# Kernel tuning notes

Measured on AMD Instinct MI355X. Metric: run time of the kernel, lower is better.

Reference implementation:

```python
import jax, jax.numpy as jnp
import numpy as np

EPS = 1e-5
SLOPE = 0.01  # LeakyReLU negative_slope

def _ln(x, g, b):
    m = jnp.mean(x, axis=-1, keepdims=True)
    v = jnp.mean((x - m) ** 2, axis=-1, keepdims=True)
    return (x - m) * jax.lax.rsqrt(v + EPS) * g + b

def _lrelu(x):
    return jnp.where(x >= 0, x, SLOPE * x)

def _s6(x, W1, b1, W2, b2, W3, b3, A):
    # x: (B, L, D); A: (D, N). Mamba-style S6 selective scan.
    Bm = x @ W2 + b2                       # (B, L, N) input-dependent B
    Cm = x @ W3 + b3                       # (B, L, N) input-dependent C
    delta = jax.nn.softplus(x @ W1 + b1)   # (B, L, D) step sizes
    dA = jnp.exp(jnp.einsum('bld,dn->bldn', delta, A))            # (B,L,D,N)
    dBx = jnp.einsum('bld,bln->bldn', delta, Bm) * x[..., None]    # (B,L,D,N) dB * x
    Bsz, L, D = x.shape
    N = A.shape[1]
    def step(h, inp):
        dA_t, dBx_t, C_t = inp
        h = dA_t * h + dBx_t                       # (B, D, N)
        return h, jnp.einsum('bn,bdn->bd', C_t, h)  # y_t: (B, D)
    xs = (jnp.transpose(dA, (1, 0, 2, 3)),
          jnp.transpose(dBx, (1, 0, 2, 3)),
          jnp.transpose(Cm, (1, 0, 2)))
    _, ys = jax.lax.scan(step, jnp.zeros((Bsz, D, N), x.dtype), xs)
    return jnp.transpose(ys, (1, 0, 2))  # (B, L, D)

def _fwd(text, audio, video, tW1, tb1, tg1, tbe1, tW2, tb2, tg2, tbe2, sW1, sb1, sW2, sb2, sW3, sb3, sA, aW1, ab1, ag1, abe1, aW2, ab2, ag2, abe2, vW1, vb1, vg1, vbe1, vW2, vb2, vg2, vbe2, cW1, cb1, cW2, cb2):
    # text branch: Linear+LN+LeakyReLU x2, Dropout(eval=identity), S6
    t = _lrelu(_ln(text @ tW1 + tb1, tg1, tbe1))
    t = _lrelu(_ln(t @ tW2 + tb2, tg2, tbe2))
    t = _s6(t, sW1, sb1, sW2, sb2, sW3, sb3, sA)
    # audio / video branches are computed but do not feed the output (as in source)
    a = _lrelu(_ln(audio @ aW1 + ab1, ag1, abe1))
    a = _lrelu(_ln(a @ aW2 + ab2, ag2, abe2))
    v = _lrelu(_ln(video @ vW1 + vb1, vg1, vbe1))
    v = _lrelu(_ln(v @ vW2 + vb2, vg2, vbe2))
    o1 = t @ cW1 + cb1
    return o1 @ cW2 + cb2  # (B, L, 2)

def setup_inputs() -> dict:
    key = jax.random.key(0)
    ks = iter(jax.random.split(key, 64))
    def W(shape, s=0.05):
        return jax.random.normal(next(ks), shape, jnp.float32) * s
    B, L = 64, 63
    d = {
        'text': jax.random.normal(next(ks), (B, L, 100), jnp.float32),
        'audio': jax.random.normal(next(ks), (B, L, 73), jnp.float32),
        'video': jax.random.normal(next(ks), (B, L, 100), jnp.float32),
        'tW1': W((100, 128)), 'tb1': jnp.zeros(128), 'tg1': jnp.ones(128), 'tbe1': jnp.zeros(128),
        'tW2': W((128, 100)), 'tb2': jnp.zeros(100), 'tg2': jnp.ones(100), 'tbe2': jnp.zeros(100),
        'sW1': W((100, 100)), 'sb1': jnp.zeros(100),
        'sW2': W((100, 300)), 'sb2': jnp.zeros(300),
        'sW3': W((100, 300)), 'sb3': jnp.zeros(300),
        'sA': jnp.full((100, 300), 1.0 / np.sqrt(300.0), jnp.float32),  # F.normalize(ones, dim=-1)
        'aW1': W((73, 256)), 'ab1': jnp.zeros(256), 'ag1': jnp.ones(256), 'abe1': jnp.zeros(256),
        'aW2': W((256, 100)), 'ab2': jnp.zeros(100), 'ag2': jnp.ones(100), 'abe2': jnp.zeros(100),
        'vW1': W((100, 256)), 'vb1': jnp.zeros(256), 'vg1': jnp.ones(256), 'vbe1': jnp.zeros(256),
        'vW2': W((256, 100)), 'vb2': jnp.zeros(100), 'vg2': jnp.ones(100), 'vbe2': jnp.zeros(100),
        'cW1': W((100, 50)), 'cb1': jnp.zeros(50),
        'cW2': W((50, 2)), 'cb2': jnp.zeros(2),
    }
    return d

def reference(text, audio, video, tW1, tb1, tg1, tbe1, tW2, tb2, tg2, tbe2, sW1, sb1, sW2, sb2, sW3, sb3, sA, aW1, ab1, ag1, abe1, aW2, ab2, ag2, abe2, vW1, vb1, vg1, vbe1, vW2, vb2, vg2, vbe2, cW1, cb1, cW2, cb2):
    return _fwd(text, audio, video, tW1, tb1, tg1, tbe1, tW2, tb2, tg2, tbe2, sW1, sb1, sW2, sb2, sW3, sb3, sA, aW1, ab1, ag1, abe1, aW2, ab2, ag2, abe2, vW1, vb1, vg1, vbe1, vW2, vb2, vg2, vbe2, cW1, cb1, cW2, cb2)
```

## Files before the change

kernel.cpp:

```cpp
#include <hip/hip_runtime.h>
#include <hip/hip_bf16.h>


typedef __hip_bfloat16 bf16;

#define BATCH 64
#define SEQ   63
#define ROWS  (BATCH * SEQ)
#define DIN   100
#define H1    128
#define DM    100
#define NS    300

__device__ __forceinline__ float2 up2(unsigned u) {
    float2 r;
    r.x = __uint_as_float(u << 16);
    r.y = __uint_as_float(u & 0xffff0000u);
    return r;
}
template<bool ISB>
__device__ __forceinline__ float LD(const void* p, int i) {
    if (ISB) return __bfloat162float(((const bf16*)p)[i]);
    else     return ((const float*)p)[i];
}
template<bool ISB>
__device__ __forceinline__ float2 LD2(const void* p, int i) {
    if (ISB) return up2(((const unsigned*)p)[i]);
    else     return ((const float2*)p)[i];
}
__device__ __forceinline__ float waveReduceSum(float v) {
#pragma unroll
    for (int off = 32; off > 0; off >>= 1) v += __shfl_xor(v, off, 64);
    return v;
}
__device__ __forceinline__ float4 waveReduceSum4(float4 v) {
#pragma unroll
    for (int off = 32; off > 0; off >>= 1) {
        const float a = __shfl_xor(v.x, off, 64);
        const float b = __shfl_xor(v.y, off, 64);
        const float c = __shfl_xor(v.z, off, 64);
        const float d = __shfl_xor(v.w, off, 64);
        v.x += a; v.y += b; v.z += c; v.w += d;
    }
    return v;
}
__device__ __forceinline__ float lrelu(float x) { return x >= 0.f ? x : 0.01f * x; }
__device__ __forceinline__ float softplusf(float x) {
    return (x > 20.f) ? x : log1pf(__expf(x));
}
__device__ __forceinline__ bool flags_uniform(const float* __restrict__ f) {
    bool u = true;
#pragma unroll
    for (int i = 0; i < 8; ++i) u &= (f[i] > 0.5f);
    return u;
}
__device__ __forceinline__ bool detect_bf16(const unsigned short* __restrict__ probe) {
    const int l = threadIdx.x & 63;
    const unsigned u0 = probe[l * 2];
    const unsigned u1 = probe[l * 2 + 1];
    const float v0 = fabsf(__uint_as_float(u0 << 16));
    const float v1 = fabsf(__uint_as_float(u1 << 16));
    const bool big = !(v0 < 1000.f) || !(v1 < 1000.f);
    const bool zero_even = (u0 == 0u);
    const unsigned long long mb = __ballot(big);
    const unsigned long long mz = __ballot(zero_even);
    return (mb == 0ULL) && (__popcll(mz) < 32);
}

template<bool ISB>
__device__ __forceinline__ void a_main(
    const void* __restrict__ text,
    const void* __restrict__ tW1, const void* __restrict__ tb1,
    const void* __restrict__ tg1, const void* __restrict__ tbe1,
    const void* __restrict__ tW2, const void* __restrict__ tb2,
    const void* __restrict__ tg2, const void* __restrict__ tbe2,
    const void* __restrict__ sW1w, const void* __restrict__ sb1,
    float* __restrict__ ddx, float* __restrict__ t2g,
    float* __restrict__ sW,
    float (&xb)[4][DIN][2], float (&t1b)[4][H1][2], float (&t2b)[4][DM][2])
{
    const int tid  = threadIdx.x;
    const int w    = tid >> 6;
    const int lane = tid & 63;
    const int r0   = blockIdx.x * 8 + w * 2;

    if (lane < 50) {
#pragma unroll
        for (int r = 0; r < 2; ++r) {
            const float2 xv = LD2<ISB>(text, (r0 + r) * 50 + lane);
            xb[w][2 * lane][r]     = xv.x;
            xb[w][2 * lane + 1][r] = xv.y;
        }
    }
    for (int i = tid; i < 6400; i += 256)
        *(float2*)&sW[2 * i] = LD2<ISB>(tW1, i);
    __syncthreads();

    const float2 b1v = LD2<ISB>(tb1, lane);
    float ax0 = b1v.x, ay0 = b1v.y, ax1 = b1v.x, ay1 = b1v.y;
#pragma unroll 10
    for (int k = 0; k < DIN; ++k) {
        const float2 wv = *(const float2*)&sW[k * 128 + 2 * lane];
        const float2 xv = *(const float2*)&xb[w][k][0];
        ax0 += xv.x * wv.x; ay0 += xv.x * wv.y;
        ax1 += xv.y * wv.x; ay1 += xv.y * wv.y;
    }
    {
        float4 red = waveReduceSum4(make_float4(
            ax0 + ay0, ax0 * ax0 + ay0 * ay0,
            ax1 + ay1, ax1 * ax1 + ay1 * ay1));
        const float m0 = red.x * (1.f / 128.f);
        const float rs0 = rsqrtf(red.y * (1.f / 128.f) - m0 * m0 + 1e-5f);
        const float m1 = red.z * (1.f / 128.f);
        const float rs1 = rsqrtf(red.w * (1.f / 128.f) - m1 * m1 + 1e-5f);
        const float2 g = LD2<ISB>(tg1, lane), be = LD2<ISB>(tbe1, lane);
        float2 v;
        v.x = lrelu((ax0 - m0) * rs0 * g.x + be.x);
        v.y = lrelu((ax1 - m1) * rs1 * g.x + be.x);
        *(float2*)&t1b[w][2 * lane][0] = v;
        v.x = lrelu((ay0 - m0) * rs0 * g.y + be.y);
        v.y = lrelu((ay1 - m1) * rs1 * g.y + be.y);
        *(float2*)&t1b[w][2 * lane + 1][0] = v;
    }
    __syncthreads();

    for (int i = tid; i < 6400; i += 256)
        *(float2*)&sW[2 * i] = LD2<ISB>(tW2, i);
    __syncthreads();

    const bool act = lane < 50;
    const int  li  = act ? lane : 0;
    const float2 b2v = LD2<ISB>(tb2, li);
    float cx0 = b2v.x, cy0 = b2v.y, cx1 = b2v.x, cy1 = b2v.y;
#pragma unroll 8
    for (int k = 0; k < H1; ++k) {
        const float2 wv = *(const float2*)&sW[k * 100 + 2 * li];
        const float2 tv = *(const float2*)&t1b[w][k][0];
        cx0 += tv.x * wv.x; cy0 += tv.x * wv.y;
        cx1 += tv.y * wv.x; cy1 += tv.y * wv.y;
    }
    float u0x, u0y, u1x, u1y;
    {
        float4 red = waveReduceSum4(act ? make_float4(
            cx0 + cy0, cx0 * cx0 + cy0 * cy0,
            cx1 + cy1, cx1 * cx1 + cy1 * cy1) : make_float4(0.f, 0.f, 0.f, 0.f));
        const float m0 = red.x * 0.01f;
        const float rs0 = rsqrtf(red.y * 0.01f - m0 * m0 + 1e-5f);
        const float m1 = red.z * 0.01f;
        const float rs1 = rsqrtf(red.w * 0.01f - m1 * m1 + 1e-5f);
        if (act) {
            const float2 g = LD2<ISB>(tg2, lane), be = LD2<ISB>(tbe2, lane);
            u0x = lrelu((cx0 - m0) * rs0 * g.x + be.x);
            u0y = lrelu((cy0 - m0) * rs0 * g.y + be.y);
            u1x = lrelu((cx1 - m1) * rs1 * g.x + be.x);
            u1y = lrelu((cy1 - m1) * rs1 * g.y + be.y);
            t2b[w][2 * lane][0] = u0x; t2b[w][2 * lane + 1][0] = u0y;
            t2b[w][2 * lane][1] = u1x; t2b[w][2 * lane + 1][1] = u1y;
            *(float2*)(t2g + (r0)     * DM + 2 * lane) = make_float2(u0x, u0y);
            *(float2*)(t2g + (r0 + 1) * DM + 2 * lane) = make_float2(u1x, u1y);
        }
    }
    __syncthreads();

    for (int i = tid; i < 5000; i += 256)
        *(float2*)&sW[2 * i] = LD2<ISB>(sW1w, i);
    __syncthreads();

    const float2 sbv = LD2<ISB>(sb1, li);
    float dA0x = sbv.x, dA0y = sbv.y, dA1x = sbv.x, dA1y = sbv.y;
#pragma unroll 10
    for (int k = 0; k < DM; ++k) {
        const float2 wv = *(const float2*)&sW[k * 100 + 2 * li];
        const float2 tv = *(const float2*)&t2b[w][k][0];
        dA0x += tv.x * wv.x; dA0y += tv.x * wv.y;
        dA1x += tv.y * wv.x; dA1y += tv.y * wv.y;
    }
    if (act) {
        float de0 = softplusf(dA0x), de1 = softplusf(dA0y);
        float4 o;
        o.x = de0; o.y = de0 * u0x; o.z = de1; o.w = de1 * u0y;
        *(float4*)(ddx + (r0) * (2 * DM) + 4 * lane) = o;
        de0 = softplusf(dA1x); de1 = softplusf(dA1y);
        o.x = de0; o.y = de0 * u1x; o.z = de1; o.w = de1 * u1y;
        *(float4*)(ddx + (r0 + 1) * (2 * DM) + 4 * lane) = o;
    }
}

template<bool ISB>
__device__ __forceinline__ void a_prep(
    const void* __restrict__ sW2, const void* __restrict__ sb2,
    const void* __restrict__ sW3, const void* __restrict__ sb3,
    float* __restrict__ M33p, float* __restrict__ k0w, float* __restrict__ sW,
    int d3)
{
    const int tid = threadIdx.x;
    const int w = tid >> 6, lane = tid & 63;
    float* W3row = sW;
    float* b2v   = sW + 320;
    float* b3v   = sW + 640;
    for (int i = tid; i < 300; i += 256) {
        W3row[i] = LD<ISB>(sW3, d3 * 300 + i);
        b2v[i]   = LD<ISB>(sb2, i);
        b3v[i]   = LD<ISB>(sb3, i);
    }
    __syncthreads();
    for (int g = 0; g < 6; ++g) {
        const int d2 = w * 25 + g * 4;
        float4 p = make_float4(0.f, 0.f, 0.f, 0.f);
#pragma unroll
        for (int rep = 0; rep < 5; ++rep) {
            const int n = lane + 64 * rep;
            if (n < 300) {
                const float w3 = W3row[n];
                p.x += LD<ISB>(sW2, (d2 + 0) * 300 + n) * w3;
                p.y += LD<ISB>(sW2, (d2 + 1) * 300 + n) * w3;
                p.z += LD<ISB>(sW2, (d2 + 2) * 300 + n) * w3;
                p.w += LD<ISB>(sW2, (d2 + 3) * 300 + n) * w3;
            }
        }
        p = waveReduceSum4(p);
        if (lane == 0) {
            M33p[d3 * 102 + d2 + 0] = p.x;
            M33p[d3 * 102 + d2 + 1] = p.y;
            M33p[d3 * 102 + d2 + 2] = p.z;
            M33p[d3 * 102 + d2 + 3] = p.w;
        }
    }
    {
        const int d2 = w * 25 + 24;
        float4 p = make_float4(0.f, 0.f, 0.f, 0.f);
#pragma unroll
        for (int rep = 0; rep < 5; ++rep) {
            const int n = lane + 64 * rep;
            if (n < 300) {
                p.x += LD<ISB>(sW2, d2 * 300 + n) * W3row[n];
                if (w == 0) p.y += W3row[n] * b2v[n];
                if (w == 1) p.y += LD<ISB>(sW2, d3 * 300 + n) * b3v[n];
                if (w == 2 && d3 == 0) p.y += b2v[n] * b3v[n];
            }
        }
        p = waveReduceSum4(p);
        if (lane == 0) {
            M33p[d3 * 102 + d2] = p.x;
            if (w == 0) M33p[d3 * 102 + 100] = p.y;
            if (w == 1) M33p[d3 * 102 + 101] = p.y;
            if (w == 2 && d3 == 0) k0w[0] = p.y;
        }
    }
}

template<bool ISB>
__device__ __forceinline__ void a_check(
    const void* __restrict__ sA, float* __restrict__ Afl,
    float* __restrict__ sW, int j)
{
    const int tid = threadIdx.x;
    const float a0 = LD<ISB>(sA, 0);
    bool ok = true;
    for (int i = j * 3750 + tid; i < (j + 1) * 3750; i += 256)
        ok &= (LD<ISB>(sA, i) == a0);
    if (tid == 0) sW[960] = 1.f;
    __syncthreads();
    if (!ok) sW[960] = 0.f;
    __syncthreads();
    if (tid == 0) Afl[j] = sW[960];
    if (j == 0 && tid == 1) Afl[8] = a0;
}

template<bool ISB>
__device__ __forceinline__ void a_mkv(
    const void* __restrict__ cW1, const void* __restrict__ cb1,
    const void* __restrict__ cW2, const void* __restrict__ cb2,
    float* __restrict__ Mkv)
{
    const int t = threadIdx.x;
    if (t < 200) {
        const int d = t >> 1, j = t & 1;
        float m = 0.f;
#pragma unroll 5
        for (int i = 0; i < 50; ++i)
            m += LD<ISB>(cW1, d * 50 + i) * LD<ISB>(cW2, 2 * i + j);
        Mkv[t] = m;
    } else if (t < 202) {
        const int j = t - 200;
        float kv = LD<ISB>(cb2, j);
#pragma unroll 5
        for (int i = 0; i < 50; ++i)
            kv += LD<ISB>(cb1, i) * LD<ISB>(cW2, 2 * i + j);
        Mkv[200 + j] = kv;
    }
}

__global__ __launch_bounds__(256) void k_A(
    const void* text,
    const void* tW1, const void* tb1, const void* tg1, const void* tbe1,
    const void* tW2, const void* tb2, const void* tg2, const void* tbe2,
    const void* sW1w, const void* sb1,
    const void* sW2, const void* sb2, const void* sW3, const void* sb3,
    const void* sA,
    const void* cW1, const void* cb1, const void* cW2, const void* cb2,
    float* ddx, float* t2g, float* Mkv, float* M33p, float* k0w, float* Afl,
    const unsigned short* probe)
{
    __shared__ __align__(16) float sW[12800];
    __shared__ __align__(16) float xb[4][DIN][2];
    __shared__ __align__(16) float t1b[4][H1][2];
    __shared__ __align__(16) float t2b[4][DM][2];
    const bool isb = detect_bf16(probe);
    const int blk = blockIdx.x;
    if (blk < 504) {
        if (isb) a_main<true >(text, tW1, tb1, tg1, tbe1, tW2, tb2, tg2, tbe2,
                               sW1w, sb1, ddx, t2g, sW, xb, t1b, t2b);
        else     a_main<false>(text, tW1, tb1, tg1, tbe1, tW2, tb2, tg2, tbe2,
                               sW1w, sb1, ddx, t2g, sW, xb, t1b, t2b);
    } else if (blk < 604) {
        if (isb) a_prep<true >(sW2, sb2, sW3, sb3, M33p, k0w, sW, blk - 504);
        else     a_prep<false>(sW2, sb2, sW3, sb3, M33p, k0w, sW, blk - 504);
    } else if (blk < 612) {
        if (isb) a_check<true >(sA, Afl, sW, blk - 604);
        else     a_check<false>(sA, Afl, sW, blk - 604);
    } else {
        if (isb) a_mkv<true >(cW1, cb1, cW2, cb2, Mkv);
        else     a_mkv<false>(cW1, cb1, cW2, cb2, Mkv);
    }
}

template<bool ISB>
__device__ __forceinline__ void gyh_impl(
    const float* __restrict__ t2g, const float* __restrict__ ddx,
    const float* __restrict__ M33p, const float* __restrict__ k0w,
    const float* __restrict__ Mkv, const float* __restrict__ Afl,
    void* __restrict__ outp,
    float* __restrict__ sT2, float* __restrict__ sM,
    float* __restrict__ sZ, float* __restrict__ sG,
    float* __restrict__ srv, float* __restrict__ sMk)
{
    const int bid = blockIdx.x;
    const int xcd = bid & 7;
    const int jj  = bid >> 3;
    const int b   = xcd * 8 + (jj >> 2);
    const int q   = jj & 3;
    const int tid = threadIdx.x;
    const int w = tid >> 6, lane = tid & 63;

    const int tmax  = (q * 16 + 15 < SEQ) ? q * 16 + 15 : SEQ - 1;
    const int srows = tmax + 1;

    for (int i = tid; i < srows * 50; i += 512) {
        const float2 v = ((const float2*)t2g)[b * 3150 + i];
        const int t = i / 50, k2 = i % 50;
        sT2[t * 102 + 2 * k2]     = v.x;
        sT2[t * 102 + 2 * k2 + 1] = v.y;
    }
    for (int i = tid; i < 5100; i += 512)
        *(float2*)&sM[2 * i] = ((const float2*)M33p)[i];
    if (tid < 202) sMk[tid] = Mkv[tid];
    __syncthreads();

    {
        const float mv0 = sM[lane * 102 + 101];
        const float mv1 = (lane < 36) ? sM[(64 + lane) * 102 + 101] : 0.f;
#pragma unroll
        for (int g = 0; g < 2; ++g) {
            float4 p;
            float acc[4];
#pragma unroll
            for (int i = 0; i < 4; ++i) {
                const int s = w * 8 + g * 4 + i;
                const int scl = (s <= tmax) ? s : 0;
                float a = sT2[scl * 102 + lane] * mv0;
                if (lane < 36) a += sT2[scl * 102 + 64 + lane] * mv1;
                acc[i] = a;
            }
            p = waveReduceSum4(make_float4(acc[0], acc[1], acc[2], acc[3]));
            if (lane == 0) {
                const int s0 = w * 8 + g * 4;
                srv[s0 + 0] = p.x; srv[s0 + 1] = p.y;
                srv[s0 + 2] = p.z; srv[s0 + 3] = p.w;
            }
        }
    }
    {
        const int l2 = (lane < 51) ? 2 * lane : 0;
        const int zr0 = w * 2, zr1 = w * 2 + 1;
        const int t0 = q * 16 + zr0;
        const int t1 = q * 16 + zr1;
        const int tc1 = (t1 <= tmax) ? t1 : tmax;
        float2 a0 = make_float2(0.f, 0.f);
        float2 a1 = make_float2(0.f, 0.f);
#pragma unroll 4
        for (int k = 0; k < 100; ++k) {
            const float2 wv = *(const float2*)&sM[k * 102 + l2];
            const float x0 = sT2[t0 * 102 + k];
            const float x1 = sT2[tc1 * 102 + k];
            a0.x += x0 * wv.x; a0.y += x0 * wv.y;
            a1.x += x1 * wv.x; a1.y += x1 * wv.y;
        }
        if (lane < 51) {
            *(float2*)&sZ[zr0 * 102 + l2] = a0;
            if (t1 <= tmax) *(float2*)&sZ[zr1 * 102 + l2] = a1;
        }
    }
    __syncthreads();

    {
        const float kz = k0w[0];
        const int sc  = (lane <= tmax) ? lane : tmax;
        const int zr0 = w * 2, zr1 = w * 2 + 1;
        const int t1  = q * 16 + zr1;
        float g0 = kz + sZ[zr0 * 102 + 100] + srv[sc];
        float g1 = kz + sZ[zr1 * 102 + 100] + srv[sc];
#pragma unroll 5
        for (int k2 = 0; k2 < 50; ++k2) {
            const float2 tv = *(const float2*)&sT2[sc * 102 + 2 * k2];
            const float2 z0 = *(const float2*)&sZ[zr0 * 102 + 2 * k2];
            const float2 z1 = *(const float2*)&sZ[zr1 * 102 + 2 * k2];
            g0 += z0.x * tv.x + z0.y * tv.y;
            g1 += z1.x * tv.x + z1.y * tv.y;
        }
        if (lane <= tmax) {
            sG[zr0 * 64 + lane] = g0;
            if (t1 <= tmax) sG[zr1 * 64 + lane] = g1;
        }
    }
    __syncthreads();

    for (int i = tid; i < srows * 100; i += 512) {
        const float2 v = ((const float2*)ddx)[b * 6300 + i];
        sT2[i] = v.x;
        sM[i]  = v.y;
    }
    __syncthreads();

    {
        const float av = Afl[8];
        if (tid < 100) {
            const int d = tid;
            float D = 0.f;
            for (int s = 0; s <= tmax; ++s) {
                D += sT2[s * 100 + d];
                const float En = __expf(-av * D);
                sM[s * 100 + d] = sM[s * 100 + d] * En;
                const int zr = s - q * 16;
                if (zr >= 0) sM[6400 + zr * 100 + d] = __expf(av * D);
            }
        }
    }
    __syncthreads();

    {
        const int li = (lane < 50) ? lane : 49;
        const float4 mk = *(const float4*)&sMk[4 * li];
        float4 oc = make_float4(0.f, 0.f, 0.f, 0.f);
#pragma unroll
        for (int r = 0; r < 2; ++r) {
            const int zr = w * 2 + r;
            const int t  = q * 16 + zr;
            float o0 = 0.f, o1 = 0.f;
            if (t < SEQ) {
                float a0 = 0.f, a1 = 0.f;
                const int nf = (t + 1) >> 1;
                const float* gp = &sG[zr * 64];
                for (int s2 = 0; s2 < nf; ++s2) {
                    const float2 g2 = *(const float2*)&gp[2 * s2];
                    const float2 v0 = *(const float2*)&sM[(2 * s2) * 100 + 2 * li];
                    const float2 v1 = *(const float2*)&sM[(2 * s2 + 1) * 100 + 2 * li];
                    a0 += g2.x * v0.x + g2.y * v1.x;
                    a1 += g2.x * v0.y + g2.y * v1.y;
                }
                if ((t & 1) == 0) {
                    const float gg = gp[t];
                    const float2 vt = *(const float2*)&sM[t * 100 + 2 * li];
                    a0 += gg * vt.x; a1 += gg * vt.y;
                }
                const float2 e2 = *(const float2*)&sM[6400 + zr * 100 + 2 * li];
                const float y0 = (lane < 50) ? e2.x * a0 : 0.f;
                const float y1 = (lane < 50) ? e2.y * a1 : 0.f;
                o0 = y0 * mk.x + y1 * mk.z;
                o1 = y0 * mk.y + y1 * mk.w;
            }
            if (r == 0) { oc.x = o0; oc.y = o1; }
            else        { oc.z = o0; oc.w = o1; }
        }
        oc = waveReduceSum4(oc);
        if (lane == 0) {
            const float kv0 = sMk[200], kv1 = sMk[201];
#pragma unroll
            for (int r = 0; r < 2; ++r) {
                const int t = q * 16 + w * 2 + r;
                if (t >= SEQ) continue;
                const int row = b * SEQ + t;
                const float o0 = (r == 0 ? oc.x : oc.z) + kv0;
                const float o1 = (r == 0 ? oc.y : oc.w) + kv1;
                if (ISB) {
                    ((bf16*)outp)[row * 2 + 0] = __float2bfloat16(o0);
                    ((bf16*)outp)[row * 2 + 1] = __float2bfloat16(o1);
                } else {
                    *(float2*)((float*)outp + row * 2) = make_float2(o0, o1);
                }
            }
        }
    }
}

__global__ __launch_bounds__(512) void k_GYH(
    const float* __restrict__ t2g, const float* __restrict__ ddx,
    const float* __restrict__ M33p, const float* __restrict__ k0w,
    const float* __restrict__ Mkv, const float* __restrict__ Afl,
    void* __restrict__ outp, const unsigned short* __restrict__ probe)
{
    __shared__ __align__(16) float sT2[6426];
    __shared__ __align__(16) float sM[10240];
    __shared__ __align__(16) float sZ[1632];
    __shared__ __align__(16) float sG[1024];
    __shared__ __align__(16) float srv[64];
    __shared__ __align__(16) float sMk[204];
    if (!flags_uniform(Afl)) return;
    if (detect_bf16(probe))
        gyh_impl<true >(t2g, ddx, M33p, k0w, Mkv, Afl, outp, sT2, sM, sZ, sG, srv, sMk);
    else
        gyh_impl<false>(t2g, ddx, M33p, k0w, Mkv, Afl, outp, sT2, sM, sZ, sG, srv, sMk);
}

template<bool ISB>
__device__ __forceinline__ float4 LD4(const void* p, int i) {
    if (ISB) {
        const uint2 u = ((const uint2*)p)[i];
        float4 r;
        r.x = __uint_as_float(u.x << 16);
        r.y = __uint_as_float(u.x & 0xffff0000u);
        r.z = __uint_as_float(u.y << 16);
        r.w = __uint_as_float(u.y & 0xffff0000u);
        return r;
    } else return ((const float4*)p)[i];
}

template<bool ISB>
__device__ __forceinline__ void b_impl(
    const float* __restrict__ t2g,
    const void* __restrict__ sW2, const void* __restrict__ sb2,
    const void* __restrict__ sW3, const void* __restrict__ sb3,
    float* __restrict__ BC, float (&sT)[DM][8])
{
    const int t  = threadIdx.x;
    const int r0 = blockIdx.x * 8;
    if (t < DM) {
#pragma unroll
        for (int r = 0; r < 8; ++r) sT[t][r] = t2g[(r0 + r) * DM + t];
    }
    __syncthreads();
    const bool isB = t < 75;
    const bool valid = t < 150;
    const int colbase = isB ? 4 * t : (valid ? 4 * (t - 75) : 0);
    const void* Wp   = isB ? sW2 : sW3;
    const void* bias = isB ? sb2 : sb3;
    const int rs4 = NS >> 2;
    const int cb4 = colbase >> 2;
    float4 acc[8];
    {
        const float4 bv = LD4<ISB>(bias, cb4);
#pragma unroll
        for (int r = 0; r < 8; ++r) acc[r] = bv;
    }
    float4 ring[4];
#pragma unroll
    for (int j = 0; j < 4; ++j) ring[j] = LD4<ISB>(Wp, j * rs4 + cb4);
    for (int kk = 0; kk < DM; kk += 4) {
#pragma unroll
        for (int j = 0; j < 4; ++j) {
            const int k = kk + j;
            const float4 wv = ring[j];
            if (k + 4 < DM) ring[j] = LD4<ISB>(Wp, (k + 4) * rs4 + cb4);
            const float4 lo = *(const float4*)&sT[k][0];
            const float4 hi = *(const float4*)&sT[k][4];
            acc[0].x += lo.x * wv.x; acc[0].y += lo.x * wv.y; acc[0].z += lo.x * wv.z; acc[0].w += lo.x * wv.w;
            acc[1].x += lo.y * wv.x; acc[1].y += lo.y * wv.y; acc[1].z += lo.y * wv.z; acc[1].w += lo.y * wv.w;
            acc[2].x += lo.z * wv.x; acc[2].y += lo.z * wv.y; acc[2].z += lo.z * wv.z; acc[2].w += lo.z * wv.w;
            acc[3].x += lo.w * wv.x; acc[3].y += lo.w * wv.y; acc[3].z += lo.w * wv.z; acc[3].w += lo.w * wv.w;
            acc[4].x += hi.x * wv.x; acc[4].y += hi.x * wv.y; acc[4].z += hi.x * wv.z; acc[4].w += hi.x * wv.w;
            acc[5].x += hi.y * wv.x; acc[5].y += hi.y * wv.y; acc[5].z += hi.y * wv.z; acc[5].w += hi.y * wv.w;
            acc[6].x += hi.z * wv.x; acc[6].y += hi.z * wv.y; acc[6].z += hi.z * wv.z; acc[6].w += hi.z * wv.w;
            acc[7].x += hi.w * wv.x; acc[7].y += hi.w * wv.y; acc[7].z += hi.w * wv.z; acc[7].w += hi.w * wv.w;
        }
    }
    if (valid) {
        const int off = isB ? 0 : 1;
#pragma unroll
        for (int r = 0; r < 8; ++r) {
            float* bp = BC + (r0 + r) * (2 * NS) + 2 * colbase + off;
            bp[0] = acc[r].x; bp[2] = acc[r].y;
            bp[4] = acc[r].z; bp[6] = acc[r].w;
        }
    }
}

__global__ __launch_bounds__(192, 1) void k_B(
    const float* t2g, const void* sW2, const void* sb2,
    const void* sW3, const void* sb3, float* BC,
    const float* Afl, const unsigned short* probe)
{
    __shared__ __align__(16) float sT[DM][8];
    if (flags_uniform(Afl)) return;
    if (detect_bf16(probe)) b_impl<true >(t2g, sW2, sb2, sW3, sb3, BC, sT);
    else                    b_impl<false>(t2g, sW2, sb2, sW3, sb3, BC, sT);
}

template<bool ISB>
__device__ __forceinline__ void scan_impl(
    const float* __restrict__ ddx, const float* __restrict__ BC,
    const void* __restrict__ sA, float* __restrict__ y,
    float (&sacc)[4][16][2][68])
{
    const int w    = threadIdx.x >> 6;
    const int lane = threadIdx.x & 63;
    const int wid  = blockIdx.x * 4 + w;
    const int b    = wid / 50;
    const int dp   = wid % 50;
    const int d0   = 2 * dp, d1 = d0 + 1;

    int nc[5]; bool nv[5];
    float A0[5], A1[5], h0[5], h1[5];
#pragma unroll
    for (int c = 0; c < 5; ++c) {
        const int n = lane + 64 * c;
        nv[c] = n < NS;
        nc[c] = nv[c] ? n : 0;
        A0[c] = nv[c] ? LD<ISB>(sA, d0 * NS + nc[c]) : 0.f;
        A1[c] = nv[c] ? LD<ISB>(sA, d1 * NS + nc[c]) : 0.f;
        h0[c] = 0.f; h1[c] = 0.f;
    }
    const float* ddp = ddx + (b * SEQ) * (2 * DM) + 4 * dp;
    const float* BCp = BC  + (b * SEQ) * (2 * NS);
    float*       yp  = y   + (b * SEQ) * DM + d0;

    float4 pdd[3];
    float2 pbc[3][5];
#pragma unroll
    for (int j = 0; j < 3; ++j) {
        pdd[j] = *(const float4*)(ddp + j * (2 * DM));
#pragma unroll
        for (int c = 0; c < 5; ++c)
            pbc[j][c] = nv[c] ? *(const float2*)(BCp + j * (2 * NS) + 2 * nc[c])
                              : make_float2(0.f, 0.f);
    }
    const int pr = lane >> 1;
    const int hh = lane & 1;
    const int sa = pr & 15;
    const int aa = pr >> 4;

#pragma unroll 3
    for (int l = 0; l < SEQ; ++l) {
        const int bi = l % 3;
        const float4 dd = pdd[bi];
        float2 bc[5];
#pragma unroll
        for (int c = 0; c < 5; ++c) bc[c] = pbc[bi][c];
        if (l + 3 < SEQ) {
            pdd[bi] = *(const float4*)(ddp + (l + 3) * (2 * DM));
#pragma unroll
            for (int c = 0; c < 5; ++c)
                pbc[bi][c] = nv[c] ? *(const float2*)(BCp + (l + 3) * (2 * NS) + 2 * nc[c])
                                   : make_float2(0.f, 0.f);
        }
        float a0 = 0.f, a1 = 0.f;
#pragma unroll
        for (int c = 0; c < 5; ++c) {
            h0[c] = __expf(dd.x * A0[c]) * h0[c] + dd.y * bc[c].x;
            a0 += bc[c].y * h0[c];
            h1[c] = __expf(dd.z * A1[c]) * h1[c] + dd.w * bc[c].x;
            a1 += bc[c].y * h1[c];
        }
        const int s = l & 15;
        sacc[w][s][0][lane] = a0;
        sacc[w][s][1][lane] = a1;

        if (s == 15 || l == SEQ - 1) {
            const int l0 = l & ~15;
            const int cs = l - l0 + 1;
            float sum = 0.f;
            if (sa < cs) {
                const float* rowp = &sacc[w][sa][aa][hh * 32];
#pragma unroll
                for (int i = 0; i < 8; ++i) {
                    const float4 v = *(const float4*)(rowp + 4 * i);
                    sum += v.x + v.y + v.z + v.w;
                }
            }
            sum += __shfl_xor(sum, 1, 64);
            if (hh == 0 && sa < cs) yp[(l0 + sa) * DM + aa] = sum;
        }
    }
}

__global__ __launch_bounds__(256) void k_scan(
    const float* ddx, const float* BC, const void* sA, float* y,
    const float* Afl, const unsigned short* probe)
{
    __shared__ __align__(16) float sacc[4][16][2][68];
    if (flags_uniform(Afl)) return;
    if (detect_bf16(probe)) scan_impl<true >(ddx, BC, sA, y, sacc);
    else                    scan_impl<false>(ddx, BC, sA, y, sacc);
}

template<bool ISB>
__device__ __forceinline__ void headf_impl(
    const float* __restrict__ y, const float* __restrict__ Mkv,
    void* __restrict__ outp)
{
    const int row = blockIdx.x * 256 + threadIdx.x;
    if (row >= ROWS) return;
    float a0 = Mkv[200], a1 = Mkv[201];
    const float* yr = y + row * DM;
#pragma unroll 4
    for (int k = 0; k < DM; ++k) {
        const float v = yr[k];
        const float2 m = *(const float2*)(Mkv + 2 * k);
        a0 += v * m.x;
        a1 += v * m.y;
    }
    if (ISB) {
        ((bf16*)outp)[row * 2 + 0] = __float2bfloat16(a0);
        ((bf16*)outp)[row * 2 + 1] = __float2bfloat16(a1);
    } else {
        *(float2*)((float*)outp + row * 2) = make_float2(a0, a1);
    }
}

__global__ __launch_bounds__(256) void k_headF(
    const float* y, const float* Mkv, void* outp,
    const float* Afl, const unsigned short* probe)
{
    if (flags_uniform(Afl)) return;
    if (detect_bf16(probe)) headf_impl<true >(y, Mkv, outp);
    else                    headf_impl<false>(y, Mkv, outp);
}

extern "C" void kernel_launch(void* const* d_in, const int* in_sizes, int n_in,
                              void* d_out, int out_size, void* d_ws, size_t ws_size,
                              hipStream_t stream)
{
    const void* text = d_in[0];
    const void* tW1  = d_in[3];
    const void* tb1  = d_in[4];
    const void* tg1  = d_in[5];
    const void* tbe1 = d_in[6];
    const void* tW2  = d_in[7];
    const void* tb2  = d_in[8];
    const void* tg2  = d_in[9];
    const void* tbe2 = d_in[10];
    const void* sW1  = d_in[11];
    const void* sb1  = d_in[12];
    const void* sW2  = d_in[13];
    const void* sb2  = d_in[14];
    const void* sW3  = d_in[15];
    const void* sb3  = d_in[16];
    const void* sA   = d_in[17];
    const void* cW1  = d_in[34];
    const void* cb1  = d_in[35];
    const void* cW2  = d_in[36];
    const void* cb2  = d_in[37];
    const unsigned short* probe = (const unsigned short*)d_in[3];

    float* ws   = (float*)d_ws;
    float* ddx  = ws;
    float* BCv  = ddx + ROWS * 2 * DM;
    float* yv   = BCv + ROWS * 2 * NS;
    float* Mkv  = yv + ROWS * DM;
    float* M33p = Mkv + 202;
    float* k0w  = M33p + 10200;
    float* Afl  = k0w + 1;
    float* t2g  = yv;

    k_A<<<613, 256, 0, stream>>>(
        text, tW1, tb1, tg1, tbe1, tW2, tb2, tg2, tbe2,
        sW1, sb1, sW2, sb2, sW3, sb3, sA,
        cW1, cb1, cW2, cb2,
        ddx, t2g, Mkv, M33p, k0w, Afl, probe);

    k_GYH<<<BATCH * 4, 512, 0, stream>>>(t2g, ddx, M33p, k0w, Mkv, Afl,
                                         d_out, probe);

    k_B<<<ROWS / 8, 192, 0, stream>>>(t2g, sW2, sb2, sW3, sb3, BCv, Afl, probe);
    k_scan<<<3200 / 4, 256, 0, stream>>>(ddx, BCv, sA, yv, Afl, probe);
    k_headF<<<(ROWS + 255) / 256, 256, 0, stream>>>(yv, Mkv, d_out, Afl, probe);
}
```

Baseline: 179.2 us.

## Prefetch ddx into registers early and parallelize the sequential cumulative scan

```diff
diff --git a/kernel.cpp b/kernel.cpp
--- a/kernel.cpp
+++ b/kernel.cpp
@@ -346,6 +346,14 @@
     const int tmax  = (q * 16 + 15 < SEQ) ? q * 16 + 15 : SEQ - 1;
     const int srows = tmax + 1;
 
+    float2 rdd[13];
+#pragma unroll
+    for (int j = 0; j < 13; ++j) {
+        const int i = tid + j * 512;
+        rdd[j] = (i < srows * 100) ? ((const float2*)ddx)[b * 6300 + i]
+                                   : make_float2(0.f, 0.f);
+    }
+
     for (int i = tid; i < srows * 50; i += 512) {
         const float2 v = ((const float2*)t2g)[b * 3150 + i];
         const int t = i / 50, k2 = i % 50;
@@ -425,19 +433,33 @@
     }
     __syncthreads();
 
-    for (int i = tid; i < srows * 100; i += 512) {
-        const float2 v = ((const float2*)ddx)[b * 6300 + i];
-        sT2[i] = v.x;
-        sM[i]  = v.y;
+#pragma unroll
+    for (int j = 0; j < 13; ++j) {
+        const int i = tid + j * 512;
+        if (i < srows * 100) {
+            sT2[i] = rdd[j].x;
+            sM[i]  = rdd[j].y;
+        }
     }
     __syncthreads();
 
     {
         const float av = Afl[8];
-        if (tid < 100) {
-            const int d = tid;
+        const int c = tid >> 7;
+        const int d = tid & 127;
+        const int L = (srows + 3) >> 2;
+        const int s0 = c * L;
+        const int s1 = (s0 + L < srows) ? s0 + L : srows;
+        if (d < 100) {
+            float Ts = 0.f;
+            for (int s = s0; s < s1; ++s) Ts += sT2[s * 100 + d];
+            sZ[c * 128 + d] = Ts;
+        }
+        __syncthreads();
+        if (d < 100) {
             float D = 0.f;
-            for (int s = 0; s <= tmax; ++s) {
+            for (int cc = 0; cc < c; ++cc) D += sZ[cc * 128 + d];
+            for (int s = s0; s < s1; ++s) {
                 D += sT2[s * 100 + d];
                 const float En = __expf(-av * D);
                 sM[s * 100 + d] = sM[s * 100 + d] * En;
```

Result: faster. 175.1 us (-2.3%).
